# Optimization experiments

Measured on AMD Instinct MI355X. Metric: run time of the kernel, lower is better.

Reference implementation:

```python
import jax, jax.numpy as jnp
import numpy as np
from jax import lax

B, LAT, NCLS, NGF, NC = 256, 100, 10, 128, 3
EPS = 1e-5


def _convt(x, w, stride, pad):
    # torch ConvTranspose2d(weight shape (Cin,Cout,k,k)) == lhs-dilated conv
    # with spatially flipped, in/out-swapped kernel and padding k-1-pad.
    k = w.shape[2]
    wt = jnp.flip(w, (2, 3)).transpose(1, 0, 2, 3)  # (Cout, Cin, k, k)
    p = k - 1 - pad
    return lax.conv_general_dilated(x, wt, (1, 1), [(p, p), (p, p)],
                                    lhs_dilation=(stride, stride),
                                    dimension_numbers=('NCHW', 'OIHW', 'NCHW'))


def _cconvt(xr, xi, wr, wi, br, bi, stride, pad):
    # complex transposed conv decomposed into 4 real convs (as torch does)
    yr = _convt(xr, wr, stride, pad) - _convt(xi, wi, stride, pad) + br[None, :, None, None]
    yi = _convt(xr, wi, stride, pad) + _convt(xi, wr, stride, pad) + bi[None, :, None, None]
    return yr, yi


def _cbn(xr, xi, grr, gri, gii, br, bi):
    # complex batchnorm: 2x2 covariance whitening over (N,H,W) + affine
    ax = (0, 2, 3)
    bc = lambda v: v[None, :, None, None]
    xr = xr - bc(xr.mean(ax))
    xi = xi - bc(xi.mean(ax))
    crr = (xr * xr).mean(ax) + EPS
    cii = (xi * xi).mean(ax) + EPS
    cri = (xr * xi).mean(ax)
    s = jnp.sqrt(crr * cii - cri * cri)          # sqrt(det)
    t = jnp.sqrt(crr + cii + 2.0 * s)            # sqrt(trace + 2 sqrt(det))
    inv = 1.0 / (s * t)
    rrr = (cii + s) * inv
    rii = (crr + s) * inv
    rri = -cri * inv
    yr = bc(rrr) * xr + bc(rri) * xi
    yi = bc(rri) * xr + bc(rii) * xi
    out_r = bc(grr) * yr + bc(gri) * yi + bc(br)
    out_i = bc(gri) * yr + bc(gii) * yi + bc(bi)
    return out_r, out_i


def _forward(noise_re, noise_im, labels, emb,
             w1r, w1i, b1r, b1i, g1rr, g1ri, g1ii, n1br, n1bi,
             w2r, w2i, b2r, b2i, g2rr, g2ri, g2ii, n2br, n2bi,
             w3r, w3i, b3r, b3i, g3rr, g3ri, g3ii, n3br, n3bi,
             w4r, w4i, b4r, b4i):
    lab = emb[labels][:, :, None, None]  # (B, NCLS, 1, 1); embedding is real
    xr = jnp.concatenate([noise_re, lab], axis=1)
    xi = jnp.concatenate([noise_im, jnp.zeros_like(lab)], axis=1)
    # 1x1 -> 4x4
    xr, xi = _cconvt(xr, xi, w1r, w1i, b1r, b1i, 1, 0)
    xr, xi = _cbn(xr, xi, g1rr, g1ri, g1ii, n1br, n1bi)
    xr, xi = jax.nn.relu(xr), jax.nn.relu(xi)  # CReLU
    # 4x4 -> 8x8
    xr, xi = _cconvt(xr, xi, w2r, w2i, b2r, b2i, 2, 1)
    xr, xi = _cbn(xr, xi, g2rr, g2ri, g2ii, n2br, n2bi)
    xr, xi = jax.nn.relu(xr), jax.nn.relu(xi)
    # 8x8 -> 16x16
    xr, xi = _cconvt(xr, xi, w3r, w3i, b3r, b3i, 2, 1)
    xr, xi = _cbn(xr, xi, g3rr, g3ri, g3ii, n3br, n3bi)
    xr, xi = jax.nn.relu(xr), jax.nn.relu(xi)
    # 16x16 -> 32x32
    xr, xi = _cconvt(xr, xi, w4r, w4i, b4r, b4i, 2, 1)
    return jnp.tanh(xr), jnp.tanh(xi)  # CTanh


def setup_inputs() -> dict:
    key = jax.random.key(0)
    ks = iter(jax.random.split(key, 40))
    rn = lambda shape, s: jax.random.normal(next(ks), shape, jnp.float32) * s
    d = {}
    d['noise_re'] = rn((B, LAT, 1, 1), 1.0)
    d['noise_im'] = rn((B, LAT, 1, 1), 1.0)
    d['labels'] = jax.random.randint(next(ks), (B,), 0, NCLS, jnp.int32)
    d['emb'] = rn((NCLS, NCLS), 1.0)
    chans = [(LAT + NCLS, NGF * 4), (NGF * 4, NGF * 2), (NGF * 2, NGF), (NGF, NC)]
    for i, (ci, co) in enumerate(chans, 1):
        d[f'w{i}r'] = rn((ci, co, 4, 4), 0.02)
        d[f'w{i}i'] = rn((ci, co, 4, 4), 0.02)
        d[f'b{i}r'] = jnp.zeros((co,), jnp.float32)
        d[f'b{i}i'] = jnp.zeros((co,), jnp.float32)
        if i < 4:
            d[f'g{i}rr'] = jnp.full((co,), 0.70710678, jnp.float32)
            d[f'g{i}ri'] = jnp.zeros((co,), jnp.float32)
            d[f'g{i}ii'] = jnp.full((co,), 0.70710678, jnp.float32)
            d[f'n{i}br'] = jnp.zeros((co,), jnp.float32)
            d[f'n{i}bi'] = jnp.zeros((co,), jnp.float32)
    return d


def reference(noise_re, noise_im, labels, emb,
              w1r, w1i, b1r, b1i, g1rr, g1ri, g1ii, n1br, n1bi,
              w2r, w2i, b2r, b2i, g2rr, g2ri, g2ii, n2br, n2bi,
              w3r, w3i, b3r, b3i, g3rr, g3ri, g3ii, n3br, n3bi,
              w4r, w4i, b4r, b4i):
    out_r, out_i = _forward(noise_re, noise_im, labels, emb,
                            w1r, w1i, b1r, b1i, g1rr, g1ri, g1ii, n1br, n1bi,
                            w2r, w2i, b2r, b2i, g2rr, g2ri, g2ii, n2br, n2bi,
                            w3r, w3i, b3r, b3i, g3rr, g3ri, g3ii, n3br, n3bi,
                            w4r, w4i, b4r, b4i)
    return out_r + 1j * out_i  # complex64 (B, NC, 32, 32)
```

## Files before the change

kernel.cpp:

```cpp
#include <hip/hip_runtime.h>
#include <hip/hip_bf16.h>
#include <math.h>

#define BATCH 256
#define LAT 100
#define NCLS 10
#define CIN0 110
#define C1 512
#define C2 256
#define C3 128
#define NCH 3
#define EPS 1e-5f
#define NCOPY 8

typedef __hip_bfloat16 bf16;
typedef short bf16x8 __attribute__((ext_vector_type(8)));
typedef float f32x4 __attribute__((ext_vector_type(4)));

__device__ __forceinline__ float b2f(bf16 v) { return __bfloat162float(v); }
__device__ __forceinline__ bf16 f2b(float v) { return __float2bfloat16(v); }
__device__ __forceinline__ float s2f(short s) {
    unsigned u = ((unsigned)(unsigned short)s) << 16;
    return __builtin_bit_cast(float, u);
}
__device__ __forceinline__ short f2s(float f) {
    bf16 b = __float2bfloat16(f);
    return *(short*)&b;
}

#define NB_W1 14336
#define NB_W2 32768
#define NB_W3 8192
#define NB_W4 256
#define NB_X0 224
#define NB_Z  36

__device__ __forceinline__ void w1prep_body(const float* wr, const float* wi, bf16* B, int idx) {
    if (idx >= 16384 * 224) return;
    int n = idx / 224, k = idx - n * 224;
    int p = n >> 10;
    int c = (n & 1023) >> 1;
    int part = n & 1;
    int pk = k >= 112; int ci = k - pk * 112;
    float v = 0.f;
    if (ci < CIN0) {
        size_t widx = ((size_t)ci * C1 + c) * 16 + p;
        float vr = wr[widx], vi = wi[widx];
        v = (part == 0) ? (pk ? -vi : vr) : (pk ? vr : vi);
    }
    B[idx] = f2b(v);
}

template<int CIN, int N>
__device__ __forceinline__ void wprep_panel_body(const float* wr, const float* wi, bf16* W,
                                                 size_t idx) {
    constexpr int TWOK = 8 * CIN, C2I = 2 * CIN;
    size_t per_cls = (size_t)2 * N * TWOK;
    if (idx >= 4 * per_cls) return;
    int cls = (int)(idx / per_cls);
    size_t r = idx - (size_t)cls * per_cls;
    size_t chunk_nb = (size_t)TWOK * 128;
    int nb = (int)(r / chunk_nb);
    int r2 = (int)(r - (size_t)nb * chunk_nb);
    int kb = r2 >> 12;
    int w = r2 & 4095;
    int f = w >> 9;
    int l = (w >> 3) & 63;
    int j = w & 7;
    int n_virt = nb * 128 + (f >> 2) * 64 + (f & 3) * 16 + (l & 15);
    int k = kb * 32 + (l >> 4) * 8 + j;
    int c = n_virt >> 1, part = n_virt & 1;
    int t = k / C2I;
    int q = k & (C2I - 1);
    int ci = q >> 1, p = q & 1;
    int py = cls >> 1, px = cls & 1;
    int a = t >> 1, e = t & 1;
    int kh = py ? (a ? 2 : 0) : (a ? 3 : 1);
    int kw = px ? (e ? 2 : 0) : (e ? 3 : 1);
    size_t widx = ((size_t)ci * N + c) * 16 + kh * 4 + kw;
    float vr = wr[widx], vi = wi[widx];
    float v = (part == 0) ? (p ? -vi : vr) : (p ? vr : vi);
    W[idx] = f2b(v);
}

__device__ __forceinline__ void wprep4_body(const float* wr, const float* wi, bf16* W, int idx) {
    if (idx >= 65536) return;
    int cls = idx >> 14, rem = idx & 16383;
    int py = cls >> 1, px = cls & 1;
    int n = rem >> 10, k = rem & 1023;
    float v = 0.f;
    if (n < NCH) {
        int t = k >> 8, q = k & 255;
        int ci = q >> 1, p = q & 1;
        int a = t >> 1, e = t & 1;
        int kh = py ? (a ? 2 : 0) : (a ? 3 : 1);
        int kw = px ? (e ? 2 : 0) : (e ? 3 : 1);
        size_t widx = ((size_t)ci * NCH + n) * 16 + kh * 4 + kw;
        v = p ? -wi[widx] : wr[widx];
    }
    W[idx] = f2b(v);
}

__device__ __forceinline__ void x0_body(const float* nre, const float* nim,
                                        const int* labels, const float* emb,
                                        bf16* A, int idx) {
    if (idx >= BATCH * 224) return;
    int b = idx / 224, k = idx - b * 224;
    int p = k >= 112; int ci = k - p * 112;
    float v = 0.f;
    if (ci < CIN0) {
        if (!p) v = (ci < LAT) ? nre[b * LAT + ci] : emb[labels[b] * NCLS + (ci - LAT)];
        else    v = (ci < LAT) ? nim[b * LAT + ci] : 0.f;
    }
    A[idx] = f2b(v);
}

__global__ void prep_combined(const float* __restrict__ w1r, const float* __restrict__ w1i,
                              const float* __restrict__ w2r, const float* __restrict__ w2i,
                              const float* __restrict__ w3r, const float* __restrict__ w3i,
                              const float* __restrict__ w4r, const float* __restrict__ w4i,
                              const float* __restrict__ nre, const float* __restrict__ nim,
                              const int* __restrict__ labels, const float* __restrict__ emb,
                              bf16* __restrict__ B1, bf16* __restrict__ W2all,
                              bf16* __restrict__ W3all, bf16* __restrict__ W4all,
                              bf16* __restrict__ x0bf, float* __restrict__ Szero) {
    int bid = blockIdx.x;
    if (bid < NB_W1) {
        w1prep_body(w1r, w1i, B1, bid * 256 + threadIdx.x);
    } else if (bid < NB_W1 + NB_W2) {
        wprep_panel_body<C1, C2>(w2r, w2i, W2all, (size_t)(bid - NB_W1) * 256 + threadIdx.x);
    } else if (bid < NB_W1 + NB_W2 + NB_W3) {
        wprep_panel_body<C2, C3>(w3r, w3i, W3all, (size_t)(bid - NB_W1 - NB_W2) * 256 + threadIdx.x);
    } else if (bid < NB_W1 + NB_W2 + NB_W3 + NB_W4) {
        wprep4_body(w4r, w4i, W4all, (bid - NB_W1 - NB_W2 - NB_W3) * 256 + threadIdx.x);
    } else if (bid < NB_W1 + NB_W2 + NB_W3 + NB_W4 + NB_X0) {
        x0_body(nre, nim, labels, emb, x0bf,
                (bid - NB_W1 - NB_W2 - NB_W3 - NB_W4) * 256 + threadIdx.x);
    } else {
        int idx = (bid - NB_W1 - NB_W2 - NB_W3 - NB_W4 - NB_X0) * 256 + threadIdx.x;
        if (idx < 35840) Szero[idx] = 0.f;
    }
}

__device__ __forceinline__ void epi_stats_flush(float* red, float* Scopy, int Cn,
                                                int cBaseGlobal, int tid, int lq,
                                                const int* clArr, float* s1,
                                                float* s2, float* sp, int isRe) {
    for (int i = tid; i < 320; i += 256) red[i] = 0.f;
    __syncthreads();
#pragma unroll
    for (int sn = 0; sn < 4; ++sn) {
        s1[sn] += __shfl_xor(s1[sn], 16, 64); s1[sn] += __shfl_xor(s1[sn], 32, 64);
        s2[sn] += __shfl_xor(s2[sn], 16, 64); s2[sn] += __shfl_xor(s2[sn], 32, 64);
        sp[sn] += __shfl_xor(sp[sn], 16, 64); sp[sn] += __shfl_xor(sp[sn], 32, 64);
    }
    if (lq == 0) {
#pragma unroll
        for (int sn = 0; sn < 4; ++sn) {
            int cl = clArr[sn];
            if (isRe) {
                atomicAdd(&red[cl * 5 + 0], s1[sn]);
                atomicAdd(&red[cl * 5 + 2], s2[sn]);
                atomicAdd(&red[cl * 5 + 4], sp[sn]);
            } else {
                atomicAdd(&red[cl * 5 + 1], s1[sn]);
                atomicAdd(&red[cl * 5 + 3], s2[sn]);
            }
        }
    }
    __syncthreads();
    for (int i = tid; i < 320; i += 256) {
        int cl = i / 5, st = i - cl * 5;
        atomicAdd(&Scopy[st * Cn + cBaseGlobal + cl], red[i]);
    }
}

__global__ __launch_bounds__(256, 1) void gemm1(
    const bf16* __restrict__ A, const bf16* __restrict__ B,
    const float* __restrict__ b1r, const float* __restrict__ b1i,
    bf16* __restrict__ Y, float* __restrict__ Sstat) {
    __shared__ short As[128][40];
    __shared__ short Bs[128][40];
    const int tid = threadIdx.x;
    const int mBase = blockIdx.x * 128, nBase = blockIdx.y * 128;
    const int wid = tid >> 6, lane = tid & 63;
    const int wm = (wid >> 1) * 64, wn = (wid & 1) * 64;
    const int lm = lane & 15, lq = lane >> 4;

    f32x4 acc[4][4] = {};

    for (int k0 = 0; k0 < 224; k0 += 32) {
#pragma unroll
        for (int it = 0; it < 2; ++it) {
            int slot = tid + it * 256;
            int row = slot >> 2, kc = (slot & 3) * 8;
            int k = k0 + kc;
            *(uint4*)(&As[row][kc]) = *(const uint4*)(A + (size_t)(mBase + row) * 224 + k);
            *(uint4*)(&Bs[row][kc]) = *(const uint4*)(B + (size_t)(nBase + row) * 224 + k);
        }
        __syncthreads();
        bf16x8 af[4], bfr[4];
#pragma unroll
        for (int s = 0; s < 4; ++s) {
            af[s]  = *(const bf16x8*)(&As[wm + s * 16 + lm][lq * 8]);
            bfr[s] = *(const bf16x8*)(&Bs[wn + s * 16 + lm][lq * 8]);
        }
#pragma unroll
        for (int sm = 0; sm < 4; ++sm)
#pragma unroll
            for (int sn = 0; sn < 4; ++sn)
                acc[sm][sn] = __builtin_amdgcn_mfma_f32_16x16x32_bf16(af[sm], bfr[sn], acc[sm][sn], 0, 0, 0);
        __syncthreads();
    }

    float s1[4] = {}, s2[4] = {}, sp[4] = {};
    int clArr[4];
#pragma unroll
    for (int sn = 0; sn < 4; ++sn) clArr[sn] = (wn + sn * 16 + lm) >> 1;
    const int part = lm & 1;

#pragma unroll
    for (int sm = 0; sm < 4; ++sm) {
#pragma unroll
        for (int v = 0; v < 4; ++v) {
            int m = mBase + wm + sm * 16 + lq * 4 + v;
#pragma unroll
            for (int sn = 0; sn < 4; ++sn) {
                int n = nBase + wn + sn * 16 + lm;
                int c = (n & 1023) >> 1;
                float bias = part ? b1i[c] : b1r[c];
                float val = acc[sm][sn][v] + bias;
                float pv = __shfl_xor(val, 1, 64);
                s1[sn] += val; s2[sn] += val * val;
                if (!part) sp[sn] += val * pv;
                Y[(size_t)m * 16384 + n] = f2b(val);
            }
        }
    }
    int copy = (blockIdx.y * gridDim.x + blockIdx.x) & (NCOPY - 1);
    epi_stats_flush((float*)As, Sstat + (size_t)copy * 5 * C1, C1,
                    (nBase & 1023) >> 1, tid, lq, clArr, s1, s2, sp, !part);
}

__global__ void bn_apply_v3(bf16* __restrict__ Y, const float* __restrict__ Scopies,
                            const float* __restrict__ grr, const float* __restrict__ gri,
                            const float* __restrict__ gii,
                            const float* __restrict__ betar, const float* __restrict__ betai,
                            int C, int total8, float invN) {
    __shared__ float coefs[6][512];
    for (int c = threadIdx.x; c < C; c += 256) {
        float sr = 0, si = 0, srr = 0, sii = 0, sri = 0;
        for (int cp = 0; cp < NCOPY; ++cp) {
            const float* S = Scopies + (size_t)cp * 5 * C;
            sr += S[c]; si += S[C + c]; srr += S[2 * C + c]; sii += S[3 * C + c]; sri += S[4 * C + c];
        }
        float mr = sr * invN, mi = si * invN;
        float crr = srr * invN - mr * mr + EPS;
        float cii = sii * invN - mi * mi + EPS;
        float cri = sri * invN - mr * mi;
        float s = sqrtf(crr * cii - cri * cri);
        float t = sqrtf(crr + cii + 2.f * s);
        float inv = 1.f / (s * t);
        float rrr = (cii + s) * inv, rii = (crr + s) * inv, rri = -cri * inv;
        float Grr = grr[c], Gri = gri[c], Gii = gii[c];
        float arr = Grr * rrr + Gri * rri, ari = Grr * rri + Gri * rii;
        float air = Gri * rrr + Gii * rri, aii = Gri * rri + Gii * rii;
        coefs[0][c] = arr; coefs[1][c] = ari;
        coefs[2][c] = betar[c] - arr * mr - ari * mi;
        coefs[3][c] = air; coefs[4][c] = aii;
        coefs[5][c] = betai[c] - air * mr - aii * mi;
    }
    __syncthreads();
    int idx = blockIdx.x * 256 + threadIdx.x;
    if (idx >= total8) return;
    size_t base = (size_t)idx * 8;
    int c0 = ((int)(base & (size_t)(2 * C - 1))) >> 1;
    bf16x8 v8 = *(const bf16x8*)(Y + base);
    bf16x8 o8;
#pragma unroll
    for (int u = 0; u < 4; ++u) {
        int c = c0 + u;
        float vr = s2f(v8[2 * u]), vi = s2f(v8[2 * u + 1]);
        o8[2 * u]     = f2s(fmaxf(coefs[0][c] * vr + coefs[1][c] * vi + coefs[2][c], 0.f));
        o8[2 * u + 1] = f2s(fmaxf(coefs[3][c] * vr + coefs[4][c] * vi + coefs[5][c], 0.f));
    }
    *(bf16x8*)(Y + base) = o8;
}

template<int CIN, int S, int N>
__global__ __launch_bounds__(256, 3) void gemm_convt_bd(
    const bf16* __restrict__ X, const bf16* __restrict__ Wall,
    const float* __restrict__ biasr, const float* __restrict__ biasi,
    bf16* __restrict__ Y, float* __restrict__ Sstat) {
    constexpr int TWOK = 8 * CIN, C2I = 2 * CIN, C2O = 2 * N, HOUT = 2 * S;
    constexpr int NSTEP = TWOK / 64;
    constexpr int CPS32 = C2I / 32;
    constexpr int LOG_CPS = (CIN == 512) ? 5 : 4;
    constexpr int GX = (BATCH * S * S) / 128;
    constexpr int GY = C2O / 128;
    constexpr int GZ = 4;
    constexpr int NWG = GX * GY * GZ;
    constexpr int CHUNK = NWG / 8;
    constexpr int NYZ = GY * GZ;
    __shared__ short As[2][2][128][40];

    const int phys = (blockIdx.z * GY + blockIdx.y) * GX + blockIdx.x;
    const int L = (phys & 7) * CHUNK + (phys >> 3);
    const int bx = L / NYZ;
    const int ryz = L - bx * NYZ;
    const int by = ryz % GY;
    const int bz = ryz / GY;

    const int cls = bz;
    const int py = cls >> 1, px = cls & 1;
    const int tid = threadIdx.x;
    const int mBase = bx * 128, nBase = by * 128;
    const int wid = tid >> 6, lane = tid & 63;
    const int wm = (wid >> 1) * 64, wn = (wid & 1) * 64;
    const int lm = lane & 15, lq = lane >> 4;
    const int dh0 = py ? 1 : 0, dh1 = py ? 0 : -1;
    const int dw0 = px ? 1 : 0, dw1 = px ? 0 : -1;

    const bf16* Wp = Wall
        + ((size_t)(cls * (C2O / 128) + by) * (TWOK / 32)) * 4096
        + ((wn >> 6) * 4) * 512 + lane * 8;

    int rowA[2], kcA[2];
    int offT[2][4];
#pragma unroll
    for (int j = 0; j < 2; ++j) {
        int slot = tid + j * 256;
        rowA[j] = slot >> 2; kcA[j] = (slot & 3) * 8;
        int m = mBase + rowA[j];
        int b = m / (S * S); int rem = m - b * (S * S);
        int i = rem / S, jj = rem % S;
#pragma unroll
        for (int t = 0; t < 4; ++t) {
            int a = t >> 1, e = t & 1;
            int ih = i + (a ? dh1 : dh0);
            int iw = jj + (e ? dw1 : dw0);
            offT[j][t] = ((unsigned)ih < (unsigned)S && (unsigned)iw < (unsigned)S)
                ? ((b * S + ih) * S + iw) * C2I : -1;
        }
    }

    auto loadA = [&](int ksn, uint4* av) {
        int kb0 = 2 * ksn;
        int t = kb0 >> LOG_CPS;
        int q0 = (kb0 & (CPS32 - 1)) << 5;
#pragma unroll
        for (int it = 0; it < 4; ++it) {
            int j = it & 1, h = it >> 1;
            int o = offT[j][t];
            uint4 v = {0u, 0u, 0u, 0u};
            if (o >= 0)
                v = *(const uint4*)(X + (size_t)o + q0 + h * 32 + kcA[j]);
            av[it] = v;
        }
    };

    f32x4 acc[4][4] = {};
    bf16x8 bA[4];

    {
        uint4 a0[4];
        loadA(0, a0);
#pragma unroll
        for (int sn = 0; sn < 4; ++sn) bA[sn] = *(const bf16x8*)(Wp + sn * 512);
#pragma unroll
        for (int it = 0; it < 4; ++it)
            *(uint4*)(&As[0][it >> 1][rowA[it & 1]][kcA[it & 1]]) = a0[it];
    }
    __syncthreads();

    for (int ks = 0; ks < NSTEP; ++ks) {
        const int cur = ks & 1;
        const bool hasNext = (ks + 1 < NSTEP);
        uint4 aS[4];
        if (hasNext) loadA(ks + 1, aS);
        bf16x8 bB[4];
        {
            const bf16* W1 = Wp + (size_t)(2 * ks + 1) * 4096;
#pragma unroll
            for (int sn = 0; sn < 4; ++sn) bB[sn] = *(const bf16x8*)(W1 + sn * 512);
        }
        {
            bf16x8 af[4];
#pragma unroll
            for (int s = 0; s < 4; ++s)
                af[s] = *(const bf16x8*)(&As[cur][0][wm + s * 16 + lm][lq * 8]);
#pragma unroll
            for (int sm = 0; sm < 4; ++sm)
#pragma unroll
                for (int sn = 0; sn < 4; ++sn)
                    acc[sm][sn] = __builtin_amdgcn_mfma_f32_16x16x32_bf16(af[sm], bA[sn], acc[sm][sn], 0, 0, 0);
        }
        if (hasNext) {
            const bf16* W2 = Wp + (size_t)(2 * ks + 2) * 4096;
#pragma unroll
            for (int sn = 0; sn < 4; ++sn) bA[sn] = *(const bf16x8*)(W2 + sn * 512);
        }
        {
            bf16x8 af[4];
#pragma unroll
            for (int s = 0; s < 4; ++s)
                af[s] = *(const bf16x8*)(&As[cur][1][wm + s * 16 + lm][lq * 8]);
#pragma unroll
            for (int sm = 0; sm < 4; ++sm)
#pragma unroll
                for (int sn = 0; sn < 4; ++sn)
                    acc[sm][sn] = __builtin_amdgcn_mfma_f32_16x16x32_bf16(af[sm], bB[sn], acc[sm][sn], 0, 0, 0);
        }
        if (hasNext) {
#pragma unroll
            for (int it = 0; it < 4; ++it)
                *(uint4*)(&As[1 - cur][it >> 1][rowA[it & 1]][kcA[it & 1]]) = aS[it];
        }
        __syncthreads();
    }

    float s1[4] = {}, s2[4] = {}, sp[4] = {};
    int clArr[4];
#pragma unroll
    for (int sn = 0; sn < 4; ++sn) clArr[sn] = (wn + sn * 16 + lm) >> 1;
    const int part = lm & 1;

#pragma unroll
    for (int sm = 0; sm < 4; ++sm) {
#pragma unroll
        for (int v = 0; v < 4; ++v) {
            int m = mBase + wm + sm * 16 + lq * 4 + v;
            int b = m / (S * S); int rem = m - b * (S * S);
            int i = rem / S, j = rem % S;
            int oh = 2 * i + py, ow = 2 * j + px;
            size_t rowoff = (size_t)((b * HOUT + oh) * HOUT + ow) * C2O;
#pragma unroll
            for (int sn = 0; sn < 4; ++sn) {
                int n = nBase + wn + sn * 16 + lm;
                int c = n >> 1;
                float bias = part ? biasi[c] : biasr[c];
                float val = acc[sm][sn][v] + bias;
                float pv = __shfl_xor(val, 1, 64);
                s1[sn] += val; s2[sn] += val * val;
                if (!part) sp[sn] += val * pv;
                Y[rowoff + n] = f2b(val);
            }
        }
    }
    int copy = L & (NCOPY - 1);
    epi_stats_flush((float*)As, Sstat + (size_t)copy * 5 * N, N,
                    nBase >> 1, tid, lq, clArr, s1, s2, sp, !part);
}

__global__ __launch_bounds__(256, 2) void conv4_mfma(
    const bf16* __restrict__ X, const bf16* __restrict__ Wall,
    const float* __restrict__ br, float* __restrict__ out) {
    constexpr int S = 16, TWOK = 1024, C2I = 256;
    constexpr int GX = 256, GZ = 4, NWG = GX * GZ, CHUNK = NWG / 8;
    __shared__ short As[256][40];
    __shared__ short Bs[16][40];

    const int phys = blockIdx.z * GX + blockIdx.x;
    const int L = (phys & 7) * CHUNK + (phys >> 3);
    const int bx = L >> 2;
    const int cls = L & 3;

    const int py = cls >> 1, px = cls & 1;
    const bf16* W = Wall + (size_t)cls * 16 * TWOK;
    const int tid = threadIdx.x;
    const int mBase = bx * 256;
    const int wid = tid >> 6, lane = tid & 63;
    const int wm = wid * 64;
    const int lm = lane & 15, lq = lane >> 4;
    const int dh0 = py ? 1 : 0, dh1 = py ? 0 : -1;
    const int dw0 = px ? 1 : 0, dw1 = px ? 0 : -1;

    int rowA[4], kcA[4];
    long offT[4][4];
#pragma unroll
    for (int it = 0; it < 4; ++it) {
        int slot = tid + it * 256;
        rowA[it] = slot >> 2; kcA[it] = (slot & 3) * 8;
        int m = mBase + rowA[it];
        int b = m >> 8; int rem = m & 255;
        int i = rem >> 4, j = rem & 15;
#pragma unroll
        for (int t = 0; t < 4; ++t) {
            int a = t >> 1, e = t & 1;
            int ih = i + (a ? dh1 : dh0);
            int iw = j + (e ? dw1 : dw0);
            offT[it][t] = ((unsigned)ih < (unsigned)S && (unsigned)iw < (unsigned)S)
                ? (long)((b * S + ih) * S + iw) * C2I : -1L;
        }
    }

    f32x4 acc[4] = {};

    for (int kb = 0; kb < TWOK / 32; ++kb) {
        int t = kb >> 3;
        int q0 = (kb & 7) << 5;
#pragma unroll
        for (int it = 0; it < 4; ++it) {
            long o = offT[it][t];
            uint4 v = {0u, 0u, 0u, 0u};
            if (o >= 0)
                v = *(const uint4*)(X + o + q0 + kcA[it]);
            *(uint4*)(&As[rowA[it]][kcA[it]]) = v;
        }
        if (tid < 64) {
            int row = tid >> 2, kc = (tid & 3) * 8;
            uint4 w = *(const uint4*)(W + (size_t)row * TWOK + kb * 32 + kc);
            *(uint4*)(&Bs[row][kc]) = w;
        }
        __syncthreads();
        bf16x8 bfr = *(const bf16x8*)(&Bs[lm][lq * 8]);
#pragma unroll
        for (int s = 0; s < 4; ++s) {
            bf16x8 af = *(const bf16x8*)(&As[wm + s * 16 + lm][lq * 8]);
            acc[s] = __builtin_amdgcn_mfma_f32_16x16x32_bf16(af, bfr, acc[s], 0, 0, 0);
        }
        __syncthreads();
    }

    int n = lm;
    if (n < NCH) {
        float bias = br[n];
#pragma unroll
        for (int s = 0; s < 4; ++s) {
#pragma unroll
            for (int v = 0; v < 4; ++v) {
                int m = mBase + wm + s * 16 + lq * 4 + v;
                int b = m >> 8; int rem = m & 255;
                int i = rem >> 4, j = rem & 15;
                int oh = 2 * i + py, ow = 2 * j + px;
                out[((size_t)(b * NCH + n) * 32 + oh) * 32 + ow] = tanhf(acc[s][v] + bias);
            }
        }
    }
}

extern "C" void kernel_launch(void* const* d_in, const int* in_sizes, int n_in,
                              void* d_out, int out_size, void* d_ws, size_t ws_size,
                              hipStream_t stream) {
    const float* noise_re = (const float*)d_in[0];
    const float* noise_im = (const float*)d_in[1];
    const int*   labels   = (const int*)d_in[2];
    const float* emb      = (const float*)d_in[3];
    const float* w1r = (const float*)d_in[4],  *w1i = (const float*)d_in[5];
    const float* b1r = (const float*)d_in[6],  *b1i = (const float*)d_in[7];
    const float* g1rr = (const float*)d_in[8], *g1ri = (const float*)d_in[9], *g1ii = (const float*)d_in[10];
    const float* n1br = (const float*)d_in[11], *n1bi = (const float*)d_in[12];
    const float* w2r = (const float*)d_in[13], *w2i = (const float*)d_in[14];
    const float* b2r = (const float*)d_in[15], *b2i = (const float*)d_in[16];
    const float* g2rr = (const float*)d_in[17], *g2ri = (const float*)d_in[18], *g2ii = (const float*)d_in[19];
    const float* n2br = (const float*)d_in[20], *n2bi = (const float*)d_in[21];
    const float* w3r = (const float*)d_in[22], *w3i = (const float*)d_in[23];
    const float* b3r = (const float*)d_in[24], *b3i = (const float*)d_in[25];
    const float* g3rr = (const float*)d_in[26], *g3ri = (const float*)d_in[27], *g3ii = (const float*)d_in[28];
    const float* n3br = (const float*)d_in[29], *n3bi = (const float*)d_in[30];
    const float* w4r = (const float*)d_in[31], *w4i = (const float*)d_in[32];
    const float* b4r = (const float*)d_in[33], *b4i = (const float*)d_in[34];

    char* ws = (char*)d_ws;
    bf16* y3cl = (bf16*)ws;
    bf16* x1cl = (bf16*)ws;
    bf16* B1    = (bf16*)(ws + 8388608);
    bf16* W2all = (bf16*)(ws + 15728640);
    bf16* y2cl  = (bf16*)(ws + 33554432);
    bf16* W3all = (bf16*)(ws + 50331648);
    bf16* x0bf  = (bf16*)(ws + 54547456);
    bf16* W4all = (bf16*)(ws + 54662144);
    float* S1 = (float*)(ws + 54793216);
    float* S2 = (float*)(ws + 54875136);
    float* S3 = (float*)(ws + 54916096);

    prep_combined<<<NB_W1 + NB_W2 + NB_W3 + NB_W4 + NB_X0 + NB_Z, 256, 0, stream>>>(
        w1r, w1i, w2r, w2i, w3r, w3i, w4r, w4i,
        noise_re, noise_im, labels, emb,
        B1, W2all, W3all, W4all, x0bf, S1);

    gemm1<<<dim3(2, 128), 256, 0, stream>>>(x0bf, B1, b1r, b1i, x1cl, S1);
    bn_apply_v3<<<2048, 256, 0, stream>>>(x1cl, S1, g1rr, g1ri, g1ii, n1br, n1bi,
                                          C1, 524288, 1.f / 4096.f);

    gemm_convt_bd<C1, 4, C2><<<dim3(32, 4, 4), 256, 0, stream>>>(x1cl, W2all, b2r, b2i, y2cl, S2);
    bn_apply_v3<<<4096, 256, 0, stream>>>(y2cl, S2, g2rr, g2ri, g2ii, n2br, n2bi,
                                          C2, 1048576, 1.f / 16384.f);

    gemm_convt_bd<C2, 8, C3><<<dim3(128, 2, 4), 256, 0, stream>>>(y2cl, W3all, b3r, b3i, y3cl, S3);
    bn_apply_v3<<<8192, 256, 0, stream>>>(y3cl, S3, g3rr, g3ri, g3ii, n3br, n3bi,
                                          C3, 2097152, 1.f / 65536.f);

    conv4_mfma<<<dim3(256, 1, 4), 256, 0, stream>>>(y3cl, W4all, b4r, (float*)d_out);
}
```

Measured before the change: 468.6 us.

## Add dedicated 8-wave layer-3 conv-transpose GEMM with direct-to-LDS async loads

Replaces the generic gemm_convt_bd launch for layer 3 with a specialized 512-thread kernel. It uses global_load_lds to stream implicit-im2col A tiles into a 4-deep swizzled LDS ring while B fragments are register double-buffered. Out-of-bounds taps point at a zeroed buffer, which the prep kernel now clears. The aim is to hide memory latency and raise MFMA utilization through deeper pipelining and larger tiles. The cost is 128KB of LDS per block (low occupancy), a fragile hand-tuned waitcnt/barrier schedule, and a hard-coded layout.

```diff
diff --git a/kernel.cpp b/kernel.cpp
--- a/kernel.cpp
+++ b/kernel.cpp
@@ -28,12 +28,18 @@
     return *(short*)&b;
 }
 
+__device__ __forceinline__ void gl_lds16(const void* g, void* l) {
+    __builtin_amdgcn_global_load_lds(
+        (__attribute__((address_space(1))) const void*)g,
+        (__attribute__((address_space(3))) void*)l, 16, 0, 0);
+}
+
 #define NB_W1 14336
 #define NB_W2 32768
 #define NB_W3 8192
 #define NB_W4 256
 #define NB_X0 224
-#define NB_Z  36
+#define NB_Z  141
 
 __device__ __forceinline__ void w1prep_body(const float* wr, const float* wi, bf16* B, int idx) {
     if (idx >= 16384 * 224) return;
@@ -123,7 +129,8 @@
                               const int* __restrict__ labels, const float* __restrict__ emb,
                               bf16* __restrict__ B1, bf16* __restrict__ W2all,
                               bf16* __restrict__ W3all, bf16* __restrict__ W4all,
-                              bf16* __restrict__ x0bf, float* __restrict__ Szero) {
+                              bf16* __restrict__ x0bf, float* __restrict__ Szero,
+                              float* __restrict__ Zb) {
     int bid = blockIdx.x;
     if (bid < NB_W1) {
         w1prep_body(w1r, w1i, B1, bid * 256 + threadIdx.x);
@@ -139,6 +146,7 @@
     } else {
         int idx = (bid - NB_W1 - NB_W2 - NB_W3 - NB_W4 - NB_X0) * 256 + threadIdx.x;
         if (idx < 35840) Szero[idx] = 0.f;
+        else if (idx < 36096) Zb[idx - 35840] = 0.f;
     }
 }
 
@@ -450,6 +458,179 @@
     int copy = L & (NCOPY - 1);
     epi_stats_flush((float*)As, Sstat + (size_t)copy * 5 * N, N,
                     nBase >> 1, tid, lq, clArr, s1, s2, sp, !part);
+}
+
+__global__ __launch_bounds__(512) void gemm3_8ph(
+    const bf16* __restrict__ X, const bf16* __restrict__ Wall,
+    const float* __restrict__ biasr, const float* __restrict__ biasi,
+    bf16* __restrict__ Y, float* __restrict__ Sstat,
+    const bf16* __restrict__ zb) {
+    constexpr int C2I = 512, C2O = 256;
+    __shared__ short As4[4][256 * 64];
+
+    const int tid = threadIdx.x;
+    const int phys = blockIdx.x;
+    const int L = (phys & 7) * 32 + (phys >> 3);
+    const int bx = L >> 2, cls = L & 3;
+    const int py = cls >> 1, px = cls & 1;
+    const int mBase = bx * 256;
+    const int wid = tid >> 6, lane = tid & 63;
+    const int wm = (wid >> 2) * 128;
+    const int wn = (wid & 3) * 64;
+    const int lm = lane & 15, lq = lane >> 4;
+    const int dh0 = py ? 1 : 0, dh1 = py ? 0 : -1;
+    const int dw0 = px ? 1 : 0, dw1 = px ? 0 : -1;
+
+    const bf16* Wb = Wall + ((size_t)(cls * 2 + (wn >> 7)) * 64) * 4096
+                     + ((wn >> 6) & 1) * 2048 + lane * 8;
+
+    const int zoff = (int)(zb - X);
+    const int c_log = (tid & 7) ^ ((tid >> 3) & 7);
+    const int rquo = tid >> 3;
+    int bI[4], iI[4], jI[4];
+#pragma unroll
+    for (int it = 0; it < 4; ++it) {
+        int m = mBase + it * 64 + rquo;
+        bI[it] = m >> 6; int rem = m & 63; iI[it] = rem >> 3; jI[it] = rem & 7;
+    }
+    const int colB0 = ((lq ^ (lm & 7)) * 8);
+    const int colB1 = (((4 + lq) ^ (lm & 7)) * 8);
+
+    f32x4 acc[8][4] = {};
+    bf16x8 bfr[2][4][2];
+
+    auto calcEO = [&](int tap, int* eo) {
+        int a = tap >> 1, e = tap & 1;
+        int dh = a ? dh1 : dh0, dw = e ? dw1 : dw0;
+#pragma unroll
+        for (int it = 0; it < 4; ++it) {
+            int ih = iI[it] + dh, iw = jI[it] + dw;
+            eo[it] = ((unsigned)ih < 8u && (unsigned)iw < 8u)
+                ? ((bI[it] * 8 + ih) * 8 + iw) * C2I + c_log * 8
+                : zoff;
+        }
+    };
+
+    int eo[4], eoN[4];
+    calcEO(0, eo);
+#pragma unroll
+    for (int p = 0; p < 4; ++p)
+        gl_lds16(X + eo[p], &As4[0][p * 4096 + wid * 512]);
+    asm volatile("" ::: "memory");
+#pragma unroll
+    for (int p = 0; p < 4; ++p) {
+        gl_lds16(X + eo[p] + 64, &As4[1][p * 4096 + wid * 512]);
+        bfr[0][p][0] = *(const bf16x8*)(Wb + p * 512);
+        bfr[0][p][1] = *(const bf16x8*)(Wb + 4096 + p * 512);
+        asm volatile("" ::: "memory");
+    }
+    asm volatile("s_waitcnt vmcnt(12)" ::: "memory");
+    __builtin_amdgcn_s_barrier();
+
+    const bf16* WnP = Wb + 8192;
+
+#pragma unroll 1
+    for (int t = 0; t < 4; ++t) {
+        calcEO(t, eo);
+        calcEO(t < 3 ? t + 1 : 3, eoN);
+#pragma unroll
+        for (int k8 = 0; k8 < 8; ++k8) {
+            const short* curBuf = As4[k8 & 3];
+            short* stgBuf = As4[(k8 + 2) & 3];
+            bf16x8 (&bcur)[4][2] = bfr[k8 & 1];
+            bf16x8 (&bnx)[4][2] = bfr[(k8 + 1) & 1];
+            const int kcol = ((k8 + 2) & 7) * 64;
+#pragma unroll
+            for (int q = 0; q < 4; ++q) {
+                asm volatile("" ::: "memory");
+                bf16x8 af[2][2];
+#pragma unroll
+                for (int r = 0; r < 2; ++r) {
+                    const short* rp = curBuf + (wm + 32 * q + r * 16 + lm) * 64;
+                    af[r][0] = *(const bf16x8*)(rp + colB0);
+                    af[r][1] = *(const bf16x8*)(rp + colB1);
+                }
+                gl_lds16(X + ((k8 < 6) ? eo[q] : eoN[q]) + kcol,
+                         &stgBuf[q * 4096 + wid * 512]);
+                bnx[q][0] = *(const bf16x8*)(WnP + q * 512);
+                bnx[q][1] = *(const bf16x8*)(WnP + 4096 + q * 512);
+                __builtin_amdgcn_s_barrier();
+                __builtin_amdgcn_s_setprio(1);
+#pragma unroll
+                for (int kc = 0; kc < 2; ++kc)
+#pragma unroll
+                    for (int r = 0; r < 2; ++r)
+#pragma unroll
+                        for (int sn = 0; sn < 4; ++sn)
+                            acc[2 * q + r][sn] = __builtin_amdgcn_mfma_f32_16x16x32_bf16(
+                                af[r][kc], bcur[sn][kc], acc[2 * q + r][sn], 0, 0, 0);
+                __builtin_amdgcn_s_setprio(0);
+                if (q == 3) asm volatile("s_waitcnt vmcnt(12)" ::: "memory");
+                __builtin_amdgcn_s_barrier();
+            }
+            WnP += 8192;
+        }
+    }
+
+    __syncthreads();
+
+    float s1[4] = {}, s2[4] = {}, sp[4] = {};
+    int clArr[4];
+#pragma unroll
+    for (int sn = 0; sn < 4; ++sn) clArr[sn] = (wn + sn * 16 + lm) >> 1;
+    const int part = lm & 1;
+
+#pragma unroll
+    for (int sm = 0; sm < 8; ++sm) {
+#pragma unroll
+        for (int v = 0; v < 4; ++v) {
+            int m = mBase + wm + sm * 16 + lq * 4 + v;
+            int b = m >> 6; int rem = m & 63;
+            int i = rem >> 3, j = rem & 7;
+            int oh = 2 * i + py, ow = 2 * j + px;
+            size_t rowoff = (size_t)((b * 16 + oh) * 16 + ow) * C2O;
+#pragma unroll
+            for (int sn = 0; sn < 4; ++sn) {
+                int n = wn + sn * 16 + lm;
+                int c = n >> 1;
+                float bias = part ? biasi[c] : biasr[c];
+                float val = acc[sm][sn][v] + bias;
+                float pv = __shfl_xor(val, 1, 64);
+                s1[sn] += val; s2[sn] += val * val;
+                if (!part) sp[sn] += val * pv;
+                Y[rowoff + n] = f2b(val);
+            }
+        }
+    }
+    float* red = (float*)(&As4[0][0]);
+    for (int i2 = tid; i2 < 640; i2 += 512) red[i2] = 0.f;
+    __syncthreads();
+#pragma unroll
+    for (int sn = 0; sn < 4; ++sn) {
+        s1[sn] += __shfl_xor(s1[sn], 16, 64); s1[sn] += __shfl_xor(s1[sn], 32, 64);
+        s2[sn] += __shfl_xor(s2[sn], 16, 64); s2[sn] += __shfl_xor(s2[sn], 32, 64);
+        sp[sn] += __shfl_xor(sp[sn], 16, 64); sp[sn] += __shfl_xor(sp[sn], 32, 64);
+    }
+    if (lq == 0) {
+#pragma unroll
+        for (int sn = 0; sn < 4; ++sn) {
+            int cl = clArr[sn];
+            if (!part) {
+                atomicAdd(&red[cl * 5 + 0], s1[sn]);
+                atomicAdd(&red[cl * 5 + 2], s2[sn]);
+                atomicAdd(&red[cl * 5 + 4], sp[sn]);
+            } else {
+                atomicAdd(&red[cl * 5 + 1], s1[sn]);
+                atomicAdd(&red[cl * 5 + 3], s2[sn]);
+            }
+        }
+    }
+    __syncthreads();
+    float* Sc = Sstat + (size_t)(L & (NCOPY - 1)) * 5 * 128;
+    for (int i2 = tid; i2 < 640; i2 += 512) {
+        int cl = i2 / 5, st = i2 - cl * 5;
+        atomicAdd(&Sc[st * 128 + cl], red[i2]);
+    }
 }
 
 __global__ __launch_bounds__(256, 2) void conv4_mfma(
@@ -573,11 +754,12 @@
     float* S1 = (float*)(ws + 54793216);
     float* S2 = (float*)(ws + 54875136);
     float* S3 = (float*)(ws + 54916096);
+    float* Zb = (float*)(ws + 54526976);
 
     prep_combined<<<NB_W1 + NB_W2 + NB_W3 + NB_W4 + NB_X0 + NB_Z, 256, 0, stream>>>(
         w1r, w1i, w2r, w2i, w3r, w3i, w4r, w4i,
         noise_re, noise_im, labels, emb,
-        B1, W2all, W3all, W4all, x0bf, S1);
+        B1, W2all, W3all, W4all, x0bf, S1, Zb);
 
     gemm1<<<dim3(2, 128), 256, 0, stream>>>(x0bf, B1, b1r, b1i, x1cl, S1);
     bn_apply_v3<<<2048, 256, 0, stream>>>(x1cl, S1, g1rr, g1ri, g1ii, n1br, n1bi,
@@ -587,7 +769,8 @@
     bn_apply_v3<<<4096, 256, 0, stream>>>(y2cl, S2, g2rr, g2ri, g2ii, n2br, n2bi,
                                           C2, 1048576, 1.f / 16384.f);
 
-    gemm_convt_bd<C2, 8, C3><<<dim3(128, 2, 4), 256, 0, stream>>>(y2cl, W3all, b3r, b3i, y3cl, S3);
+    gemm3_8ph<<<dim3(256), 512, 0, stream>>>(y2cl, W3all, b3r, b3i, y3cl, S3,
+                                             (const bf16*)Zb);
     bn_apply_v3<<<8192, 256, 0, stream>>>(y3cl, S3, g3rr, g3ri, g3ii, n3br, n3bi,
                                           C3, 2097152, 1.f / 65536.f);
 
```

Result: slower. 530.4 us (+13.2%).
